# Kernel tuning notes

Hardware: AMD Instinct MI355X
Metric: run time of the kernel (lower is better)

Reference implementation:

```python
import jax, jax.numpy as jnp
import numpy as np

NUM_USERS, NUM_ITEMS, NUM_GROUPS = 100000, 50000, 20000
D = 64
B, M = 16384, 50


def setup_inputs() -> dict:
    key = jax.random.key(0)
    ks = jax.random.split(key, 16)
    inp = {
        "group_inputs": jax.random.randint(ks[0], (B,), 0, NUM_GROUPS),
        "item_inputs": jax.random.randint(ks[1], (B,), 0, NUM_ITEMS),
        "member_ids": jax.random.randint(ks[2], (B, M), 0, NUM_USERS),
        "member_lengths": jax.random.randint(ks[3], (B,), 0, M),
        # embedding tables (xavier-ish scale)
        "user_table": jax.random.normal(ks[4], (NUM_USERS, D), jnp.float32) * 0.05,
        "item_table": jax.random.normal(ks[5], (NUM_ITEMS, D), jnp.float32) * 0.05,
        "group_table": jax.random.normal(ks[6], (NUM_GROUPS, D), jnp.float32) * 0.05,
        # attention MLP: 2D -> 16 -> 1
        "att_w1": jax.random.normal(ks[7], (2 * D, 16), jnp.float32) * 0.1,
        "att_b1": jnp.zeros((16,), jnp.float32),
        "att_w2": jax.random.normal(ks[8], (16, 1), jnp.float32) * 0.1,
        "att_b2": jnp.zeros((1,), jnp.float32),
        # predict MLP: 3D -> 8 -> 1
        "pred_w1": jax.random.normal(ks[9], (3 * D, 8), jnp.float32) * 0.1,
        "pred_b1": jnp.zeros((8,), jnp.float32),
        "pred_w2": jax.random.normal(ks[10], (8, 1), jnp.float32) * 0.1,
        "pred_b2": jnp.zeros((1,), jnp.float32),
    }
    return inp


def reference(group_inputs, item_inputs, member_ids, member_lengths,
              user_table, item_table, group_table,
              att_w1, att_b1, att_w2, att_b2,
              pred_w1, pred_b1, pred_w2, pred_b2):
    # mask: at least one valid member per group
    mask = jnp.arange(M)[None, :] <= member_lengths[:, None]          # [B, M] bool
    mem_e = user_table[member_ids]                                    # [B, M, D]
    item_e = item_table[item_inputs]                                  # [B, D]

    # attention over members: concat(member, item) -> 16 -> 1
    gi = jnp.concatenate(
        [mem_e, jnp.broadcast_to(item_e[:, None, :], mem_e.shape)], axis=-1)  # [B, M, 2D]
    h = jax.nn.relu(jnp.einsum('bmk,kh->bmh', gi, att_w1) + att_b1)   # [B, M, 16]
    scores = (jnp.einsum('bmh,ho->bmo', h, att_w2) + att_b2)[..., 0]  # [B, M]
    scores = jnp.where(mask, scores, -jnp.inf)
    at_wt = jax.nn.softmax(scores, axis=-1)                           # [B, M]

    g_att = jnp.einsum('bm,bmd->bd', at_wt, mem_e)                    # [B, D]
    g = g_att + group_table[group_inputs]                             # [B, D]

    elem = g * item_e
    new_e = jnp.concatenate([elem, g, item_e], axis=-1)               # [B, 3D]
    ph = jax.nn.relu(new_e @ pred_w1 + pred_b1)                       # [B, 8]
    y = jax.nn.sigmoid(ph @ pred_w2 + pred_b2)                        # [B, 1]
    return y
```

## Files before the change

kernel.cpp:

```cpp
#include <hip/hip_runtime.h>
#include <math.h>

constexpr int MM = 50;
constexpr int DD = 64;
constexpr int HH = 16;
constexpr int PH = 8;
constexpr int WPB = 4;
constexpr int RST = 72;

typedef _Float16 half4_t  __attribute__((ext_vector_type(4)));
typedef _Float16 half8_t  __attribute__((ext_vector_type(8)));
typedef float    float4_t __attribute__((ext_vector_type(4)));

__global__ __launch_bounds__(256) void agree_mfma(
    const int* __restrict__ group_inputs,
    const int* __restrict__ item_inputs,
    const int* __restrict__ member_ids,
    const int* __restrict__ member_lengths,
    const float* __restrict__ user_table,
    const float* __restrict__ item_table,
    const float* __restrict__ group_table,
    const float* __restrict__ att_w1,
    const float* __restrict__ att_b1,
    const float* __restrict__ att_w2,
    const float* __restrict__ att_b2,
    const float* __restrict__ pred_w1,
    const float* __restrict__ pred_b1,
    const float* __restrict__ pred_w2,
    const float* __restrict__ pred_b2,
    float* __restrict__ out,
    int B)
{
    __shared__ _Float16 rows [WPB][64][RST];
    __shared__ int      idbuf[WPB][64];
    __shared__ float    wt   [WPB][64];

    const int lane = threadIdx.x & 63;
    const int wv   = threadIdx.x >> 6;
    const int b    = blockIdx.x * WPB + wv;
    if (b >= B) return;

    const int my_m  = (lane < MM) ? lane : (MM - 1);
    const int my_id = member_ids[b * MM + my_m];
    const int len      = member_lengths[b];
    const int item_idx = item_inputs[b];
    const int gid      = group_inputs[b];

    const float item_d = item_table[(unsigned)(item_idx * DD + lane)];
    const float grp_d  = group_table[(unsigned)(gid * DD + lane)];

    idbuf[wv][lane] = my_id;

    const int h = lane & 15;
    const int q = lane >> 4;
    half4_t bfrag[4];
    #pragma unroll
    for (int s = 0; s < 4; ++s) {
        #pragma unroll
        for (int e = 0; e < 4; ++e) {
            const int k = s * 16 + q * 4 + e;
            bfrag[s][e] = (_Float16)att_w1[k * HH + h];
        }
    }
    const float w2h = att_w2[h];
    const float b2  = att_b2[0];

    const int gi = lane >> 3;
    const int gj = lane & 7;
    __builtin_amdgcn_s_waitcnt(0);
    int ids[8];
    #pragma unroll
    for (int c = 0; c < 8; ++c) ids[c] = idbuf[wv][c * 8 + gi];
    #pragma unroll
    for (int c = 0; c < 8; ++c) {
        const float4* rp =
            (const float4*)(user_table + (size_t)(unsigned)ids[c] * DD + gj * 8);
        const float4 a = rp[0];
        const float4 d = rp[1];
        half8_t hv;
        hv[0] = (_Float16)a.x;  hv[1] = (_Float16)a.y;
        hv[2] = (_Float16)a.z;  hv[3] = (_Float16)a.w;
        hv[4] = (_Float16)d.x;  hv[5] = (_Float16)d.y;
        hv[6] = (_Float16)d.z;  hv[7] = (_Float16)d.w;
        *(half8_t*)&rows[wv][c * 8 + gi][gj * 8] = hv;
    }

    float hb[HH];
    {
        const float* w1b = att_w1 + (size_t)(DD + lane) * HH;
        #pragma unroll
        for (int j = 0; j < HH; ++j) hb[j] = item_d * w1b[j];
        #pragma unroll
        for (int off = 32; off > 0; off >>= 1) {
            #pragma unroll
            for (int j = 0; j < HH; ++j) hb[j] += __shfl_xor(hb[j], off, 64);
        }
        #pragma unroll
        for (int j = 0; j < HH; ++j) hb[j] += att_b1[j];
    }
    float ibh = hb[0];
    #pragma unroll
    for (int j = 1; j < HH; ++j) ibh = (h == j) ? hb[j] : ibh;

    __builtin_amdgcn_s_waitcnt(0);
    float4_t acc[4] = {{0.f,0.f,0.f,0.f}, {0.f,0.f,0.f,0.f},
                       {0.f,0.f,0.f,0.f}, {0.f,0.f,0.f,0.f}};
    #pragma unroll
    for (int s = 0; s < 4; ++s) {
        #pragma unroll
        for (int t = 0; t < 4; ++t) {
            const half4_t a =
                *(const half4_t*)&rows[wv][t * 16 + h][s * 16 + q * 4];
            acc[t] = __builtin_amdgcn_mfma_f32_16x16x16f16(a, bfrag[s],
                                                           acc[t], 0, 0, 0);
        }
    }

    float sc[4][4];
    #pragma unroll
    for (int t = 0; t < 4; ++t) {
        #pragma unroll
        for (int r = 0; r < 4; ++r) {
            float v = fmaxf(acc[t][r] + ibh, 0.0f) * w2h;
            v += __shfl_xor(v, 1, 64);
            v += __shfl_xor(v, 2, 64);
            v += __shfl_xor(v, 4, 64);
            v += __shfl_xor(v, 8, 64);
            const int m = t * 16 + q * 4 + r;
            const bool vmask = (m < MM) && (m <= len);
            sc[t][r] = vmask ? (v + b2) : -INFINITY;
        }
    }

    float mx = -INFINITY;
    #pragma unroll
    for (int t = 0; t < 4; ++t)
        #pragma unroll
        for (int r = 0; r < 4; ++r) mx = fmaxf(mx, sc[t][r]);
    mx = fmaxf(mx, __shfl_xor(mx, 16, 64));
    mx = fmaxf(mx, __shfl_xor(mx, 32, 64));

    float ew[4][4];
    float lsum = 0.0f;
    #pragma unroll
    for (int t = 0; t < 4; ++t) {
        #pragma unroll
        for (int r = 0; r < 4; ++r) {
            ew[t][r] = __expf(sc[t][r] - mx);
            lsum += ew[t][r];
        }
    }
    lsum += __shfl_xor(lsum, 16, 64);
    lsum += __shfl_xor(lsum, 32, 64);
    const float inv = 1.0f / lsum;

    if (h == 0) {
        #pragma unroll
        for (int t = 0; t < 4; ++t)
            #pragma unroll
            for (int r = 0; r < 4; ++r)
                wt[wv][t * 16 + q * 4 + r] = ew[t][r] * inv;
    }
    __builtin_amdgcn_s_waitcnt(0);

    const int mcnt = (len < MM - 1 ? len : MM - 1) + 1;
    float g = 0.0f;
    #pragma unroll 4
    for (int m = 0; m < mcnt; ++m)
        g = fmaf(wt[wv][m], (float)rows[wv][m][lane], g);
    g += grp_d;

    const float elem = g * item_d;
    float p[PH];
    {
        const float* pa = pred_w1 + (size_t)lane * PH;
        const float* pb = pred_w1 + (size_t)(DD + lane) * PH;
        const float* pc = pred_w1 + (size_t)(2 * DD + lane) * PH;
        #pragma unroll
        for (int jj = 0; jj < PH; ++jj)
            p[jj] = fmaf(elem, pa[jj], fmaf(g, pb[jj], item_d * pc[jj]));
    }
    #pragma unroll
    for (int off = 32; off > 0; off >>= 1) {
        #pragma unroll
        for (int jj = 0; jj < PH; ++jj) p[jj] += __shfl_xor(p[jj], off, 64);
    }

    if (lane == 0) {
        float acc2 = pred_b2[0];
        #pragma unroll
        for (int jj = 0; jj < PH; ++jj)
            acc2 = fmaf(fmaxf(p[jj] + pred_b1[jj], 0.0f), pred_w2[jj], acc2);
        out[b] = 1.0f / (1.0f + __expf(-acc2));
    }
}

extern "C" void kernel_launch(void* const* d_in, const int* in_sizes, int n_in,
                              void* d_out, int out_size, void* d_ws, size_t ws_size,
                              hipStream_t stream) {
    const int*   group_inputs   = (const int*)d_in[0];
    const int*   item_inputs    = (const int*)d_in[1];
    const int*   member_ids     = (const int*)d_in[2];
    const int*   member_lengths = (const int*)d_in[3];
    const float* user_table     = (const float*)d_in[4];
    const float* item_table     = (const float*)d_in[5];
    const float* group_table    = (const float*)d_in[6];
    const float* att_w1         = (const float*)d_in[7];
    const float* att_b1         = (const float*)d_in[8];
    const float* att_w2         = (const float*)d_in[9];
    const float* att_b2         = (const float*)d_in[10];
    const float* pred_w1        = (const float*)d_in[11];
    const float* pred_b1        = (const float*)d_in[12];
    const float* pred_w2        = (const float*)d_in[13];
    const float* pred_b2        = (const float*)d_in[14];
    float* out = (float*)d_out;

    const int B = in_sizes[0];
    (void)d_ws; (void)ws_size;

    const int blocks = (B + WPB - 1) / WPB;
    agree_mfma<<<blocks, 256, 0, stream>>>(
        group_inputs, item_inputs, member_ids, member_lengths,
        user_table, item_table, group_table,
        att_w1, att_b1, att_w2, att_b2,
        pred_w1, pred_b1, pred_w2, pred_b2,
        out, B);
}
```

Before: 166.0 us.

## Skip gathers and MFMA tiles for masked members, prefetch rows into registers

The user_table gather now fetches only the 8-row chunks covering valid members (up to len), and MFMA tiles and score reductions are skipped for 16-member tiles beyond the valid count. Member ids are broadcast with a wavefront shuffle instead of going through an LDS buffer. The gathered rows are held in registers across the item-bias computation before being converted and stored to LDS, so the loads overlap that work. This raises register pressure. Rows past the valid range stay uninitialized in LDS, which is harmless only while their MFMA outputs are never used, and the explicit waitcnts were removed.

New measurement: 154.9 us. -6.6%, faster.

```diff
diff --git a/kernel.cpp b/kernel.cpp
--- a/kernel.cpp
+++ b/kernel.cpp
@@ -31,9 +31,8 @@
     float* __restrict__ out,
     int B)
 {
-    __shared__ _Float16 rows [WPB][64][RST];
-    __shared__ int      idbuf[WPB][64];
-    __shared__ float    wt   [WPB][64];
+    __shared__ _Float16 rows[WPB][64][RST];
+    __shared__ float    wt  [WPB][64];
 
     const int lane = threadIdx.x & 63;
     const int wv   = threadIdx.x >> 6;
@@ -49,7 +48,23 @@
     const float item_d = item_table[(unsigned)(item_idx * DD + lane)];
     const float grp_d  = group_table[(unsigned)(gid * DD + lane)];
 
-    idbuf[wv][lane] = my_id;
+    const int mcnt = (len < MM - 1 ? len : MM - 1) + 1;
+    const int gch  = (mcnt + 7) >> 3;
+    const int nt   = (mcnt + 15) >> 4;
+
+    const int gi = lane >> 3;
+    const int gj = lane & 7;
+    float4 ga[7], gd[7];
+    #pragma unroll
+    for (int c = 0; c < 7; ++c) {
+        if (c < gch) {
+            const int id = __shfl(my_id, c * 8 + gi, 64);
+            const float4* rp =
+                (const float4*)(user_table + (size_t)(unsigned)id * DD + gj * 8);
+            ga[c] = rp[0];
+            gd[c] = rp[1];
+        }
+    }
 
     const int h = lane & 15;
     const int q = lane >> 4;
@@ -65,26 +80,6 @@
     const float w2h = att_w2[h];
     const float b2  = att_b2[0];
 
-    const int gi = lane >> 3;
-    const int gj = lane & 7;
-    __builtin_amdgcn_s_waitcnt(0);
-    int ids[8];
-    #pragma unroll
-    for (int c = 0; c < 8; ++c) ids[c] = idbuf[wv][c * 8 + gi];
-    #pragma unroll
-    for (int c = 0; c < 8; ++c) {
-        const float4* rp =
-            (const float4*)(user_table + (size_t)(unsigned)ids[c] * DD + gj * 8);
-        const float4 a = rp[0];
-        const float4 d = rp[1];
-        half8_t hv;
-        hv[0] = (_Float16)a.x;  hv[1] = (_Float16)a.y;
-        hv[2] = (_Float16)a.z;  hv[3] = (_Float16)a.w;
-        hv[4] = (_Float16)d.x;  hv[5] = (_Float16)d.y;
-        hv[6] = (_Float16)d.z;  hv[7] = (_Float16)d.w;
-        *(half8_t*)&rows[wv][c * 8 + gi][gj * 8] = hv;
-    }
-
     float hb[HH];
     {
         const float* w1b = att_w1 + (size_t)(DD + lane) * HH;
@@ -102,33 +97,51 @@
     #pragma unroll
     for (int j = 1; j < HH; ++j) ibh = (h == j) ? hb[j] : ibh;
 
-    __builtin_amdgcn_s_waitcnt(0);
+    #pragma unroll
+    for (int c = 0; c < 7; ++c) {
+        if (c < gch) {
+            half8_t hv;
+            hv[0] = (_Float16)ga[c].x;  hv[1] = (_Float16)ga[c].y;
+            hv[2] = (_Float16)ga[c].z;  hv[3] = (_Float16)ga[c].w;
+            hv[4] = (_Float16)gd[c].x;  hv[5] = (_Float16)gd[c].y;
+            hv[6] = (_Float16)gd[c].z;  hv[7] = (_Float16)gd[c].w;
+            *(half8_t*)&rows[wv][c * 8 + gi][gj * 8] = hv;
+        }
+    }
+
     float4_t acc[4] = {{0.f,0.f,0.f,0.f}, {0.f,0.f,0.f,0.f},
                        {0.f,0.f,0.f,0.f}, {0.f,0.f,0.f,0.f}};
     #pragma unroll
-    for (int s = 0; s < 4; ++s) {
-        #pragma unroll
-        for (int t = 0; t < 4; ++t) {
-            const half4_t a =
-                *(const half4_t*)&rows[wv][t * 16 + h][s * 16 + q * 4];
-            acc[t] = __builtin_amdgcn_mfma_f32_16x16x16f16(a, bfrag[s],
-                                                           acc[t], 0, 0, 0);
+    for (int t = 0; t < 4; ++t) {
+        if (t < nt) {
+            #pragma unroll
+            for (int s = 0; s < 4; ++s) {
+                const half4_t a =
+                    *(const half4_t*)&rows[wv][t * 16 + h][s * 16 + q * 4];
+                acc[t] = __builtin_amdgcn_mfma_f32_16x16x16f16(a, bfrag[s],
+                                                               acc[t], 0, 0, 0);
+            }
         }
     }
 
     float sc[4][4];
     #pragma unroll
     for (int t = 0; t < 4; ++t) {
-        #pragma unroll
-        for (int r = 0; r < 4; ++r) {
-            float v = fmaxf(acc[t][r] + ibh, 0.0f) * w2h;
-            v += __shfl_xor(v, 1, 64);
-            v += __shfl_xor(v, 2, 64);
-            v += __shfl_xor(v, 4, 64);
-            v += __shfl_xor(v, 8, 64);
-            const int m = t * 16 + q * 4 + r;
-            const bool vmask = (m < MM) && (m <= len);
-            sc[t][r] = vmask ? (v + b2) : -INFINITY;
+        if (t < nt) {
+            #pragma unroll
+            for (int r = 0; r < 4; ++r) {
+                float v = fmaxf(acc[t][r] + ibh, 0.0f) * w2h;
+                v += __shfl_xor(v, 1, 64);
+                v += __shfl_xor(v, 2, 64);
+                v += __shfl_xor(v, 4, 64);
+                v += __shfl_xor(v, 8, 64);
+                const int m = t * 16 + q * 4 + r;
+                const bool vmask = (m < MM) && (m <= len);
+                sc[t][r] = vmask ? (v + b2) : -INFINITY;
+            }
+        } else {
+            #pragma unroll
+            for (int r = 0; r < 4; ++r) sc[t][r] = -INFINITY;
         }
     }
 
@@ -161,9 +174,7 @@
             for (int r = 0; r < 4; ++r)
                 wt[wv][t * 16 + q * 4 + r] = ew[t][r] * inv;
     }
-    __builtin_amdgcn_s_waitcnt(0);
-
-    const int mcnt = (len < MM - 1 ? len : MM - 1) + 1;
+
     float g = 0.0f;
     #pragma unroll 4
     for (int m = 0; m < mcnt; ++m)
```
